# Kernel optimization log

Hardware: AMD Instinct MI355X
Metric: run time of the kernel (lower is better)

Reference implementation:

```python
import jax, jax.numpy as jnp
import numpy as np

C = 128        # in_channels
N = 80000      # nodes per type (user, item)
E = 1000000    # edges per relation
L = 400000     # link labels


def _evolve_gcn(x_src, edge_index, n_dst, p, W0, Wih, Whh, bih, bhh):
    """EvolveGCNH layer: TopK pooling -> 1-step GRU weight evolution -> GCN."""
    # TopK pooling: score = x @ p / ||p||, keep top C nodes, gate by tanh(score)
    score = x_src @ p / (jnp.linalg.norm(p) + 1e-16)          # [N_src]
    top_vals, top_idx = jax.lax.top_k(score, x_src.shape[1])   # k = C
    X_tilde = x_src[top_idx] * jnp.tanh(top_vals)[:, None]     # [C, C]
    # One GRU step: 'batch' dim = C rows of X_tilde, hidden = current weight W0
    gi = X_tilde @ Wih.T + bih                                 # [C, 3C]
    gh = W0 @ Whh.T + bhh                                      # [C, 3C]
    i_r, i_z, i_n = jnp.split(gi, 3, axis=1)
    h_r, h_z, h_n = jnp.split(gh, 3, axis=1)
    r = jax.nn.sigmoid(i_r + h_r)
    z = jax.nn.sigmoid(i_z + h_z)
    n = jnp.tanh(i_n + r * h_n)
    W = (1.0 - z) * n + z * W0                                 # evolved weight [C, C]
    # GCN propagation with symmetric degree norm, no self loops
    xw = x_src @ W                                             # [N_src, C]
    row, col = edge_index[0], edge_index[1]
    ones = jnp.ones(row.shape[0], dtype=xw.dtype)
    deg_src = jax.ops.segment_sum(ones, row, num_segments=x_src.shape[0])
    deg_dst = jax.ops.segment_sum(ones, col, num_segments=n_dst)
    inv_s = jnp.where(deg_src > 0, jax.lax.rsqrt(jnp.maximum(deg_src, 1.0)), 0.0)
    inv_d = jnp.where(deg_dst > 0, jax.lax.rsqrt(jnp.maximum(deg_dst, 1.0)), 0.0)
    norm = inv_s[row] * inv_d[col]                             # [E]
    return jax.ops.segment_sum(xw[row] * norm[:, None], col, num_segments=n_dst)


def setup_inputs() -> dict:
    key = jax.random.key(0)
    ks = jax.random.split(key, 20)
    f = lambda i, shape, s: jax.random.normal(ks[i], shape, dtype=jnp.float32) * s
    s_w = 1.0 / np.sqrt(C)
    return {
        "x_user": f(0, (N, C), 1.0),
        "x_item": f(1, (N, C), 1.0),
        "edge_ui": jax.random.randint(ks[2], (2, E), 0, N),
        "edge_iu": jax.random.randint(ks[3], (2, E), 0, N),
        "edge_label_index": jax.random.randint(ks[4], (2, L), 0, N),
        "p_ui": f(5, (C,), s_w),
        "W0_ui": f(6, (C, C), s_w),
        "Wih_ui": f(7, (3 * C, C), s_w),
        "Whh_ui": f(8, (3 * C, C), s_w),
        "bih_ui": f(9, (3 * C,), s_w),
        "bhh_ui": f(10, (3 * C,), s_w),
        "p_iu": f(11, (C,), s_w),
        "W0_iu": f(12, (C, C), s_w),
        "Wih_iu": f(13, (3 * C, C), s_w),
        "Whh_iu": f(14, (3 * C, C), s_w),
        "bih_iu": f(15, (3 * C,), s_w),
        "bhh_iu": f(16, (3 * C,), s_w),
        "W_post": f(17, (C, 2), s_w),
        "b_post": f(18, (2,), s_w),
    }


def reference(x_user, x_item, edge_ui, edge_iu, edge_label_index,
              p_ui, W0_ui, Wih_ui, Whh_ui, bih_ui, bhh_ui,
              p_iu, W0_iu, Wih_iu, Whh_iu, bih_iu, bhh_iu,
              W_post, b_post):
    # HeteroConv: one EvolveGCNH per relation, outputs grouped by dst node type
    h_item = jax.nn.relu(_evolve_gcn(x_user, edge_ui, x_item.shape[0],
                                     p_ui, W0_ui, Wih_ui, Whh_ui, bih_ui, bhh_ui))
    h_user = jax.nn.relu(_evolve_gcn(x_item, edge_iu, x_user.shape[0],
                                     p_iu, W0_iu, Wih_iu, Whh_iu, bih_iu, bhh_iu))
    # Link scorer: gather endpoints, hadamard, linear(C->2), sum over last dim
    h_src = h_user[edge_label_index[0]]                        # [L, C]
    h_dst = h_item[edge_label_index[1]]                        # [L, C]
    h = (h_src * h_dst) @ W_post + b_post                      # [L, 2]
    return jnp.sum(h, axis=-1)                                 # [L]
```

## Files before the change

kernel.cpp:

```cpp
#include <hip/hip_runtime.h>
#include <hip/hip_fp16.h>

constexpr int KC    = 128;
constexpr int NBLK  = 2048;
constexpr int CAPA  = 1024;
constexpr int CBITS = 10;
constexpr int CSZ   = 1 << CBITS;
constexpr int NBCM  = 192;

using half8   = __attribute__((ext_vector_type(8))) _Float16;
using float4v = __attribute__((ext_vector_type(4))) float;

__device__ __forceinline__ unsigned fkey(float s) {
  unsigned u = __float_as_uint(s);
  return (u & 0x80000000u) ? ~u : (u | 0x80000000u);
}

__global__ __launch_bounds__(256) void m1_cnt_scores(
    const int* __restrict__ eui, const int* __restrict__ eiu,
    unsigned* __restrict__ cnts, int* __restrict__ deg_src,
    const float* __restrict__ xu, const float* __restrict__ xi,
    const float* __restrict__ pu, const float* __restrict__ pi,
    float* __restrict__ scores, unsigned* __restrict__ hist,
    __half* __restrict__ x16,
    int E, int N, int NBC, int chunk) {
  __shared__ unsigned hD[4 * NBCM];
  int t = threadIdx.x;
  if (blockIdx.x < NBLK) {
    int blk = blockIdx.x, w = t >> 6;
    for (int b = t; b < 4 * NBCM; b += 256) hD[b] = 0;
    __syncthreads();
    int lo = blk * chunk, hi = min(2 * E, lo + chunk);
    for (int i = lo + t; i < hi; i += 256) {
      int rel = i >= E;
      const int* e = rel ? eiu : eui;
      int j = i - rel * E;
      atomicAdd(&hD[w * NBCM + ((rel * N + e[E + j]) >> CBITS)], 1u);
      atomicAdd(&deg_src[rel * N + e[j]], 1);
    }
    __syncthreads();
    for (int b = t; b < NBC; b += 256)
      cnts[(size_t)blk * NBC + b] =
          hD[b] + hD[NBCM + b] + hD[2 * NBCM + b] + hD[3 * NBCM + b];
  } else {
    int gw = (blockIdx.x - NBLK) * 8 + (t >> 5);
    if (gw >= 2 * N) return;
    int lane = t & 31;
    int rel = gw >= N;
    int r = gw - rel * N;
    const float* x = rel ? xi : xu;
    const float* p = rel ? pi : pu;
    float4 xv = ((const float4*)(x + (size_t)r * KC))[lane];
    float4 pv = ((const float4*)p)[lane];
    __half2 h0 = __floats2half2_rn(xv.x, xv.y);
    __half2 h1 = __floats2half2_rn(xv.z, xv.w);
    uint2 u; u.x = *(unsigned*)&h0; u.y = *(unsigned*)&h1;
    ((uint2*)(x16 + (size_t)gw * KC))[lane] = u;
    float s = xv.x * pv.x + xv.y * pv.y + xv.z * pv.z + xv.w * pv.w;
#pragma unroll
    for (int off = 16; off; off >>= 1) s += __shfl_down(s, off, 32);
    if (lane == 0) {
      scores[gw] = s;
      atomicAdd(&hist[rel * 65536 + (fkey(s) >> 16)], 1u);
    }
  }
}

__global__ __launch_bounds__(1024) void m2_thresh_scan1(
    const unsigned* __restrict__ cnts, unsigned* __restrict__ sc,
    unsigned* __restrict__ bsum, const unsigned* __restrict__ hist,
    unsigned* __restrict__ ctrl, int NTOT, int NBC) {
  __shared__ __align__(16) unsigned smem[1024 + 64 + 2];
  int t = threadIdx.x;
  if (blockIdx.x < 2) {
    const unsigned* h = hist + blockIdx.x * 65536;
    unsigned* c = ctrl + blockIdx.x * 8;
    unsigned* csum = smem;
    unsigned* bs = smem + 1024;
    unsigned s = 0;
    int hi = 65536 - 64 * t;
    for (int b = hi - 64; b < hi; ++b) s += h[b];
    csum[t] = s;
    __syncthreads();
    for (int off = 1; off < 1024; off <<= 1) {
      unsigned add = (t >= off) ? csum[t - off] : 0;
      __syncthreads();
      csum[t] += add;
      __syncthreads();
    }
    unsigned above = (t == 0) ? 0u : csum[t - 1];
    if (csum[t] >= 128u && above < 128u) { smem[1088] = (unsigned)t; smem[1089] = above; }
    __syncthreads();
    int chi = 65536 - 64 * (int)smem[1088];
    unsigned s_above = smem[1089];
    if (t < 64) bs[t] = h[chi - 1 - t];
    __syncthreads();
    if (t < 64) {
      unsigned v = bs[t], cum = v;
#pragma unroll
      for (int off = 1; off < 64; off <<= 1) {
        unsigned u = __shfl_up(cum, off, 64);
        if (t >= off) cum += u;
      }
      unsigned prev = cum - v;
      if (s_above + cum >= 128u && s_above + prev < 128u)
        c[0] = (unsigned)(chi - 1 - t);
    }
  } else {
    int vb = blockIdx.x - 2;
    unsigned* sh = smem;
    int li = vb * 1024 + t;
    unsigned v = 0;
    if (li < NTOT) {
      int b = li >> 11, blk = li & (NBLK - 1);
      v = cnts[(size_t)blk * NBC + b];
    }
    sh[t] = v; __syncthreads();
    for (int off = 1; off < 1024; off <<= 1) {
      unsigned add = (t >= off) ? sh[t - off] : 0;
      __syncthreads();
      sh[t] += add;
      __syncthreads();
    }
    if (li < NTOT) sc[li] = sh[t] - v;
    if (t == 1023) bsum[vb] = sh[1023];
  }
}

__global__ __launch_bounds__(512) void m3_scan2_compact(
    unsigned* __restrict__ bsum, int nb,
    const float* __restrict__ scores, unsigned* __restrict__ ctrl,
    int* __restrict__ cand_idx, float* __restrict__ cand_val, int N) {
  if (blockIdx.x == 0) {
    __shared__ unsigned sh[512];
    int t = threadIdx.x;
    unsigned v = (t < nb) ? bsum[t] : 0;
    sh[t] = v; __syncthreads();
    for (int off = 1; off < 512; off <<= 1) {
      unsigned add = (t >= off) ? sh[t - off] : 0;
      __syncthreads();
      sh[t] += add;
      __syncthreads();
    }
    if (t < nb) bsum[t] = sh[t] - v;
  } else {
    int i = (blockIdx.x - 1) * 512 + threadIdx.x;
    if (i >= 2 * N) return;
    int rel = i >= N;
    float s = scores[i];
    if ((fkey(s) >> 16) >= ctrl[rel * 8]) {
      unsigned pos = atomicAdd(&ctrl[rel * 8 + 1], 1u);
      if (pos < 2048u) {
        cand_idx[rel * 2048 + pos] = i - rel * N;
        cand_val[rel * 2048 + pos] = s;
      }
    }
  }
}

__global__ __launch_bounds__(256) void m4_topk_part(
    const int* __restrict__ eui, const int* __restrict__ eiu,
    const unsigned* __restrict__ cnts, const unsigned* __restrict__ sc,
    const unsigned* __restrict__ bsum,
    unsigned* __restrict__ recsD,
    const unsigned* __restrict__ ctrl,
    const int* __restrict__ cand_idx, const float* __restrict__ cand_val,
    const float* __restrict__ pu, const float* __restrict__ pi,
    int* __restrict__ top_idx, float* __restrict__ top_tanh,
    int E, int N, int NBC, int chunk) {
  __shared__ __align__(16) char smem[16896];
  int t = threadIdx.x;
  if (blockIdx.x < 2) {
    float* vals = (float*)smem;
    int*   idxs = (int*)(smem + 8192);
    float* red  = (float*)(smem + 16384);
    int rel = blockIdx.x;
    const float* p = rel ? pi : pu;
    int n = (int)ctrl[rel * 8 + 1]; if (n > 2048) n = 2048;
    for (int i = t; i < n; i += 256) {
      vals[i] = cand_val[rel * 2048 + i];
      idxs[i] = cand_idx[rel * 2048 + i];
    }
    if (t < 128) { float pv = p[t]; red[t] = pv * pv; }
    __syncthreads();
    for (int off = 64; off; off >>= 1) {
      if (t < off) red[t] += red[t + off];
      __syncthreads();
    }
    float pn = sqrtf(red[0]) + 1e-16f;
    for (int c = t; c < n; c += 256) {
      float v = vals[c]; int id = idxs[c];
      int rank = 0;
      for (int j = 0; j < n; ++j) {
        float vj = vals[j];
        rank += (vj > v) || (vj == v && idxs[j] < id);
      }
      if (rank < KC) {
        top_idx[rel * KC + rank] = id;
        top_tanh[rel * KC + rank] = tanhf(v / pn);
      }
    }
  } else {
    unsigned* scn    = (unsigned*)smem;
    unsigned* curD   = (unsigned*)(smem + 1024);
    unsigned* deltaD = (unsigned*)(smem + 2048);
    unsigned* stageD = (unsigned*)(smem + 3072);
    unsigned char* bktD = (unsigned char*)(smem + 7168);
    int blk = blockIdx.x - 2;
    unsigned v = (t < NBC) ? cnts[(size_t)blk * NBC + t] : 0;
    scn[t] = v; __syncthreads();
    for (int off = 1; off < 256; off <<= 1) {
      unsigned add = (t >= off) ? scn[t - off] : 0;
      __syncthreads();
      scn[t] += add;
      __syncthreads();
    }
    if (t < NBC) {
      unsigned exc = scn[t] - v;
      curD[t] = exc;
      int li = t * NBLK + blk;
      deltaD[t] = sc[li] + bsum[li >> 10] - exc;
    }
    __syncthreads();
    int lo = blk * chunk, hi = min(2 * E, lo + chunk);
    for (int i = lo + t; i < hi; i += 256) {
      int rel = i >= E;
      const int* e = rel ? eiu : eui;
      int j = i - rel * E;
      int src_g = rel * N + e[j];
      int dst_g = rel * N + e[E + j];
      int bD = dst_g >> CBITS;
      unsigned pD = atomicAdd(&curD[bD], 1u);
      stageD[pD] = (unsigned)src_g | ((unsigned)(dst_g & (CSZ - 1)) << 18);
      bktD[pD] = (unsigned char)bD;
    }
    __syncthreads();
    int cnt = hi - lo;
    for (int j = t; j < cnt; j += 256)
      recsD[deltaD[bktD[j]] + j] = stageD[j];
  }
}

__global__ __launch_bounds__(1024) void m5_refine_gru(
    const unsigned* __restrict__ sc, const unsigned* __restrict__ bsum,
    const unsigned* __restrict__ recsD,
    int* __restrict__ ssrc, int* __restrict__ deg_dst, int* __restrict__ endp,
    const float* __restrict__ xu, const float* __restrict__ xi,
    const int* __restrict__ top_idx, const float* __restrict__ top_tanh,
    const float* __restrict__ W0u, const float* __restrict__ W0i,
    const float* __restrict__ Wihu, const float* __restrict__ Wihi,
    const float* __restrict__ Whhu, const float* __restrict__ Whhi,
    const float* __restrict__ bihu, const float* __restrict__ bihi,
    const float* __restrict__ bhhu, const float* __restrict__ bhhi,
    __half* __restrict__ Wt,
    int E, int NBC, int N2) {
  __shared__ __align__(16) char smem[8256];
  int t = threadIdx.x;
  if ((int)blockIdx.x < NBC) {
    unsigned* hist = (unsigned*)smem;
    unsigned* cur  = (unsigned*)(smem + 4096);
    unsigned* t16  = (unsigned*)(smem + 8192);
    int c = blockIdx.x;
    int liLo = c * NBLK;
    int lo = (int)(sc[liLo] + bsum[liLo >> 10]);
    int hi;
    if (c + 1 < NBC) {
      int liHi = (c + 1) * NBLK;
      hi = (int)(sc[liHi] + bsum[liHi >> 10]);
    } else hi = 2 * E;
    hist[t] = 0;
    __syncthreads();
    for (int j = lo + t; j < hi; j += 1024)
      atomicAdd(&hist[recsD[j] >> 18], 1u);
    __syncthreads();
    unsigned v = hist[t];
    unsigned inc = v;
#pragma unroll
    for (int off = 1; off < 64; off <<= 1) {
      unsigned u = __shfl_up(inc, off, 64);
      if ((t & 63) >= off) inc += u;
    }
    int w = t >> 6;
    if ((t & 63) == 63) t16[w] = inc;
    __syncthreads();
    unsigned wbase = 0;
    for (int j = 0; j < 16; ++j) if (j < w) wbase += t16[j];
    unsigned exc = wbase + inc - v;
    cur[t] = exc;
    int node = c * CSZ + t;
    if (node < N2) {
      deg_dst[node] = (int)v;
      endp[node] = lo + (int)(exc + v);
    }
    __syncthreads();
    for (int j = lo + t; j < hi; j += 1024) {
      unsigned rec = recsD[j];
      unsigned pos = atomicAdd(&cur[rec >> 18], 1u);
      ssrc[lo + (int)pos] = (int)(rec & 0x3FFFFu);
    }
  } else {
    int gb = blockIdx.x - NBC;
    int rel = gb >> 7, c = gb & 127;
    const float* x   = rel ? xi   : xu;
    const float* W0  = rel ? W0i  : W0u;
    const float* Wih = rel ? Wihi : Wihu;
    const float* Whh = rel ? Whhi : Whhu;
    const float* bih = rel ? bihi : bihu;
    const float* bhh = rel ? bhhi : bhhu;
    float* xt = (float*)smem;
    float* w0 = (float*)(smem + 512);
    if (t < KC) {
      xt[t] = x[(size_t)top_idx[rel * KC + c] * KC + t] * top_tanh[rel * KC + c];
      w0[t] = W0[c * KC + t];
    }
    __syncthreads();
    if (t >= KC) return;
    int k = t;
    float gir = bih[k], giz = bih[KC + k], gin = bih[2 * KC + k];
    float ghr = bhh[k], ghz = bhh[KC + k], ghn = bhh[2 * KC + k];
    const float* wr = Wih + (size_t)k * KC;
    const float* wz = Wih + (size_t)(KC + k) * KC;
    const float* wn = Wih + (size_t)(2 * KC + k) * KC;
    const float* vr = Whh + (size_t)k * KC;
    const float* vz = Whh + (size_t)(KC + k) * KC;
    const float* vn = Whh + (size_t)(2 * KC + k) * KC;
    for (int j = 0; j < KC; ++j) {
      float xj = xt[j], hj = w0[j];
      gir += xj * wr[j]; giz += xj * wz[j]; gin += xj * wn[j];
      ghr += hj * vr[j]; ghz += hj * vz[j]; ghn += hj * vn[j];
    }
    float r = 1.f / (1.f + expf(-(gir + ghr)));
    float z = 1.f / (1.f + expf(-(giz + ghz)));
    float nn = tanhf(gin + r * ghn);
    float w = (1.f - z) * nn + z * w0[k];
    Wt[(size_t)rel * KC * KC + (size_t)k * KC + c] = __float2half_rn(w);
  }
}

__global__ __launch_bounds__(256) void k_gemm(const __half* __restrict__ x16,
                                              const __half* __restrict__ Wt,
                                              const int* __restrict__ deg_src,
                                              __half* __restrict__ xw, int N) {
  __shared__ __half Ws[KC * KC];
  __shared__ __half outs[64 * 136];
  int rel = (blockIdx.x * 64) >= N;
  int t = threadIdx.x;
  const uint4* wg = (const uint4*)(Wt + (size_t)rel * KC * KC);
#pragma unroll
  for (int i = 0; i < 8; ++i)
    ((uint4*)Ws)[t + 256 * i] = wg[t + 256 * i];
  __syncthreads();
  int wid = t >> 6, lane = t & 63;
  int l15 = lane & 15, quad = lane >> 4;
  int row0 = blockIdx.x * 64 + wid * 16;
  half8 a[4];
  const __half* xrow = x16 + (size_t)(row0 + l15) * KC + quad * 8;
#pragma unroll
  for (int ks = 0; ks < 4; ++ks) a[ks] = *(const half8*)(xrow + ks * 32);
  float4v acc[8];
#pragma unroll
  for (int nt = 0; nt < 8; ++nt) {
    acc[nt] = (float4v){0.f, 0.f, 0.f, 0.f};
#pragma unroll
    for (int ks = 0; ks < 4; ++ks) {
      half8 b = *(const half8*)&Ws[(nt * 16 + l15) * KC + ks * 32 + quad * 8];
      acc[nt] = __builtin_amdgcn_mfma_f32_16x16x32_f16(a[ks], b, acc[nt], 0, 0, 0);
    }
  }
  float scv[4];
#pragma unroll
  for (int r = 0; r < 4; ++r) {
    int dg = deg_src[row0 + quad * 4 + r];
    scv[r] = dg > 0 ? rsqrtf((float)dg) : 0.f;
  }
  __half* ob = outs + (size_t)wid * 16 * 136;
#pragma unroll
  for (int nt = 0; nt < 8; ++nt)
#pragma unroll
    for (int r = 0; r < 4; ++r)
      ob[(quad * 4 + r) * 136 + nt * 16 + l15] = __float2half_rn(acc[nt][r] * scv[r]);
  __syncthreads();
  size_t gbase = (size_t)blockIdx.x * 64 * KC;
#pragma unroll
  for (int i = 0; i < 4; ++i) {
    int idx = t + 256 * i;
    int rr = idx >> 4, cc = idx & 15;
    *(uint4*)(xw + gbase + (size_t)rr * KC + cc * 8) =
        *(const uint4*)(outs + (size_t)rr * 136 + cc * 8);
  }
}

__global__ void k_agg(const __half* __restrict__ xw, const int* __restrict__ ssrc,
                      const int* __restrict__ endp, const int* __restrict__ deg_dst,
                      __half* __restrict__ h, int n2) {
  int gw = (int)((blockIdx.x * blockDim.x + threadIdx.x) >> 6);
  if (gw >= n2) return;
  int lane = threadIdx.x & 63;
  int q = lane >> 4, l16 = lane & 15;
  int d = deg_dst[gw];
  int end = endp[gw], start = end - d;
  __half2 z = __floats2half2_rn(0.f, 0.f);
  __half2 a0[4], a1[4], a2[4], a3[4];
#pragma unroll
  for (int k = 0; k < 4; ++k) { a0[k] = z; a1[k] = z; a2[k] = z; a3[k] = z; }
  for (int i = start + q; i < end; i += 16) {
    int i1 = i + 4, i2 = i + 8, i3 = i + 12;
    bool b1 = i1 < end, b2 = i2 < end, b3 = i3 < end;
    int r0 = ssrc[i], r1, r2, r3;
    if (b1) r1 = ssrc[i1];
    if (b2) r2 = ssrc[i2];
    if (b3) r3 = ssrc[i3];
    uint4 u0 = ((const uint4*)(xw + (size_t)r0 * KC))[l16];
    uint4 u1, u2, u3;
    if (b1) u1 = ((const uint4*)(xw + (size_t)r1 * KC))[l16];
    if (b2) u2 = ((const uint4*)(xw + (size_t)r2 * KC))[l16];
    if (b3) u3 = ((const uint4*)(xw + (size_t)r3 * KC))[l16];
    {
      const __half2* p = (const __half2*)&u0;
#pragma unroll
      for (int k = 0; k < 4; ++k) a0[k] = __hadd2(a0[k], p[k]);
    }
    if (b1) {
      const __half2* p = (const __half2*)&u1;
#pragma unroll
      for (int k = 0; k < 4; ++k) a1[k] = __hadd2(a1[k], p[k]);
    }
    if (b2) {
      const __half2* p = (const __half2*)&u2;
#pragma unroll
      for (int k = 0; k < 4; ++k) a2[k] = __hadd2(a2[k], p[k]);
    }
    if (b3) {
      const __half2* p = (const __half2*)&u3;
#pragma unroll
      for (int k = 0; k < 4; ++k) a3[k] = __hadd2(a3[k], p[k]);
    }
  }
  float f[8];
#pragma unroll
  for (int k = 0; k < 4; ++k) {
    float2 x0 = __half22float2(a0[k]);
    float2 x1 = __half22float2(a1[k]);
    float2 x2 = __half22float2(a2[k]);
    float2 x3 = __half22float2(a3[k]);
    f[2 * k]     = (x0.x + x1.x) + (x2.x + x3.x);
    f[2 * k + 1] = (x0.y + x1.y) + (x2.y + x3.y);
  }
#pragma unroll
  for (int k = 0; k < 8; ++k) {
    f[k] += __shfl_xor(f[k], 16, 64);
    f[k] += __shfl_xor(f[k], 32, 64);
  }
  if (q == 0) {
    float invd = d > 0 ? rsqrtf((float)d) : 0.f;
    __half2 pk[4];
#pragma unroll
    for (int k = 0; k < 4; ++k)
      pk[k] = __floats2half2_rn(fmaxf(f[2 * k] * invd, 0.f),
                                fmaxf(f[2 * k + 1] * invd, 0.f));
    uint4 u;
    u.x = *(unsigned*)&pk[0]; u.y = *(unsigned*)&pk[1];
    u.z = *(unsigned*)&pk[2]; u.w = *(unsigned*)&pk[3];
    ((uint4*)(h + (size_t)gw * KC))[l16] = u;
  }
}

__global__ void k_links(const __half* __restrict__ h,
                        const int* __restrict__ srcs, const int* __restrict__ dsts,
                        const float* __restrict__ Wp, const float* __restrict__ bp,
                        float* __restrict__ out, int L, int N) {
  int tid = blockIdx.x * blockDim.x + threadIdx.x;
  int lane = threadIdx.x & 63;
  int q = lane >> 4, l16 = lane & 15;
  int gq = (tid >> 6) * 4 + q;
  int nq = (int)((gridDim.x * blockDim.x) >> 6) * 4;
  float w8[8];
#pragma unroll
  for (int k = 0; k < 4; ++k) {
    float4 w = ((const float4*)Wp)[l16 * 4 + k];
    w8[2 * k] = w.x + w.y; w8[2 * k + 1] = w.z + w.w;
  }
  float bs = bp[0] + bp[1];
  const __half* hu = h + (size_t)N * KC;
  for (int li = gq; li < L; li += nq) {
    int s = srcs[li], dd = dsts[li];
    uint4 ua = ((const uint4*)(hu + (size_t)s * KC))[l16];
    uint4 ub = ((const uint4*)(h + (size_t)dd * KC))[l16];
    const __half2* pa = (const __half2*)&ua;
    const __half2* pb = (const __half2*)&ub;
    float acc = 0.f;
#pragma unroll
    for (int k = 0; k < 4; ++k) {
      float2 fa = __half22float2(pa[k]);
      float2 fb = __half22float2(pb[k]);
      acc += fa.x * fb.x * w8[2 * k] + fa.y * fb.y * w8[2 * k + 1];
    }
#pragma unroll
    for (int off = 8; off; off >>= 1) acc += __shfl_xor(acc, off, 64);
    if (l16 == 0) out[li] = acc + bs;
  }
}

extern "C" void kernel_launch(void* const* d_in, const int* in_sizes, int n_in,
                              void* d_out, int out_size, void* d_ws, size_t ws_size,
                              hipStream_t stream) {
  const float* x_user = (const float*)d_in[0];
  const float* x_item = (const float*)d_in[1];
  const int*   edge_ui = (const int*)d_in[2];
  const int*   edge_iu = (const int*)d_in[3];
  const int*   elab    = (const int*)d_in[4];
  const float* p_ui   = (const float*)d_in[5];
  const float* W0_ui  = (const float*)d_in[6];
  const float* Wih_ui = (const float*)d_in[7];
  const float* Whh_ui = (const float*)d_in[8];
  const float* bih_ui = (const float*)d_in[9];
  const float* bhh_ui = (const float*)d_in[10];
  const float* p_iu   = (const float*)d_in[11];
  const float* W0_iu  = (const float*)d_in[12];
  const float* Wih_iu = (const float*)d_in[13];
  const float* Whh_iu = (const float*)d_in[14];
  const float* bih_iu = (const float*)d_in[15];
  const float* bhh_iu = (const float*)d_in[16];
  const float* W_post = (const float*)d_in[17];
  const float* b_post = (const float*)d_in[18];
  const int N = in_sizes[0] / KC;
  const int E = in_sizes[2] / 2;
  const int L = in_sizes[4] / 2;
  const int N2 = 2 * N;
  const int NBC = (N2 + CSZ - 1) >> CBITS;
  const int chunk = (2 * E + NBLK - 1) / NBLK;
  const int NTOT = NBC * NBLK;
  const int SCB = (NTOT + 1023) / 1024;

  char* wsp = (char*)d_ws;
  auto carve = [&](size_t bytes) -> void* {
    void* p = (void*)wsp;
    wsp += (bytes + 255) & ~(size_t)255;
    return p;
  };
  const size_t histB = 2 * 65536 * 4;
  const size_t zBytes = histB + 256 + (size_t)N2 * 4;
  char*     zbase    = (char*)carve(zBytes);
  unsigned* hist     = (unsigned*)zbase;
  unsigned* ctrl     = (unsigned*)(zbase + histB);
  int*      deg_src  = (int*)(zbase + histB + 256);
  __half*   x16      = (__half*)carve((size_t)N2 * KC * 2);
  __half*   xw       = (__half*)carve((size_t)N2 * KC * 2);
  __half*   h        = (__half*)carve((size_t)N2 * KC * 2);
  float*    scores   = (float*)carve((size_t)N2 * 4);
  int*      cand_idx = (int*)carve(2 * 2048 * 4);
  float*    cand_val = (float*)carve(2 * 2048 * 4);
  int*      top_idx  = (int*)carve(2 * KC * 4);
  float*    top_tanh = (float*)carve(2 * KC * 4);
  __half*   Wt16     = (__half*)carve(2 * KC * KC * 2);
  unsigned* cnts     = (unsigned*)carve((size_t)NTOT * 4);
  unsigned* sc       = (unsigned*)carve((size_t)NTOT * 4);
  unsigned* bsum     = (unsigned*)carve((size_t)SCB * 4);
  unsigned* recsD    = (unsigned*)carve((size_t)2 * E * 4);
  int*      ssrc     = (int*)carve((size_t)2 * E * 4);
  int*      deg_dst  = (int*)carve((size_t)N2 * 4);
  int*      endp     = (int*)carve((size_t)N2 * 4);

  hipMemsetAsync(zbase, 0, zBytes, stream);

  const int SBLK = (N2 + 7) / 8;
  m1_cnt_scores<<<NBLK + SBLK, 256, 0, stream>>>(edge_ui, edge_iu, cnts, deg_src,
                                                 x_user, x_item, p_ui, p_iu,
                                                 scores, hist, x16,
                                                 E, N, NBC, chunk);
  m2_thresh_scan1<<<2 + SCB, 1024, 0, stream>>>(cnts, sc, bsum, hist, ctrl,
                                                NTOT, NBC);
  m3_scan2_compact<<<1 + (N2 + 511) / 512, 512, 0, stream>>>(bsum, SCB, scores, ctrl,
                                                             cand_idx, cand_val, N);
  m4_topk_part<<<2 + NBLK, 256, 0, stream>>>(edge_ui, edge_iu, cnts, sc, bsum,
                                             recsD, ctrl, cand_idx, cand_val,
                                             p_ui, p_iu, top_idx, top_tanh,
                                             E, N, NBC, chunk);
  m5_refine_gru<<<NBC + 2 * KC, 1024, 0, stream>>>(sc, bsum, recsD, ssrc,
                                                   deg_dst, endp,
                                                   x_user, x_item, top_idx, top_tanh,
                                                   W0_ui, W0_iu, Wih_ui, Wih_iu,
                                                   Whh_ui, Whh_iu, bih_ui, bih_iu,
                                                   bhh_ui, bhh_iu, Wt16,
                                                   E, NBC, N2);
  k_gemm<<<N2 / 64, 256, 0, stream>>>(x16, Wt16, deg_src, xw, N);
  k_agg<<<(N2 + 3) / 4, 256, 0, stream>>>(xw, ssrc, endp, deg_dst, h, N2);
  k_links<<<2048, 256, 0, stream>>>(h, elab, elab + L, W_post, b_post,
                                    (float*)d_out, L, N);
}
```

Baseline: 458.4 us.

## Compute source degrees via bucketed partition instead of global atomics

Replaces the 2M global atomicAdds into deg_src with a second counting-sort partition keyed by source bucket. Block histograms are scanned alongside the destination ones, 16-bit local source ids are scattered into recsS, and per-bucket shared-memory histograms in m5 then write deg_src directly. This removes contended global atomics and the memset of deg_src. In exchange it adds an extra scan pass, an extra 4MB scatter write and readback, and more shared memory in m4.

Result: faster. 396.5 us (-13.5%).

```diff
diff --git a/kernel.cpp b/kernel.cpp
--- a/kernel.cpp
+++ b/kernel.cpp
@@ -18,17 +18,17 @@
 
 __global__ __launch_bounds__(256) void m1_cnt_scores(
     const int* __restrict__ eui, const int* __restrict__ eiu,
-    unsigned* __restrict__ cnts, int* __restrict__ deg_src,
+    unsigned* __restrict__ cnts,
     const float* __restrict__ xu, const float* __restrict__ xi,
     const float* __restrict__ pu, const float* __restrict__ pi,
     float* __restrict__ scores, unsigned* __restrict__ hist,
     __half* __restrict__ x16,
-    int E, int N, int NBC, int chunk) {
-  __shared__ unsigned hD[4 * NBCM];
+    int E, int N, int NBC, int chunk, int NTOT) {
+  __shared__ unsigned hD[4 * NBCM], hS[4 * NBCM];
   int t = threadIdx.x;
   if (blockIdx.x < NBLK) {
     int blk = blockIdx.x, w = t >> 6;
-    for (int b = t; b < 4 * NBCM; b += 256) hD[b] = 0;
+    for (int b = t; b < 4 * NBCM; b += 256) { hD[b] = 0; hS[b] = 0; }
     __syncthreads();
     int lo = blk * chunk, hi = min(2 * E, lo + chunk);
     for (int i = lo + t; i < hi; i += 256) {
@@ -36,12 +36,15 @@
       const int* e = rel ? eiu : eui;
       int j = i - rel * E;
       atomicAdd(&hD[w * NBCM + ((rel * N + e[E + j]) >> CBITS)], 1u);
-      atomicAdd(&deg_src[rel * N + e[j]], 1);
-    }
-    __syncthreads();
-    for (int b = t; b < NBC; b += 256)
+      atomicAdd(&hS[w * NBCM + ((rel * N + e[j]) >> CBITS)], 1u);
+    }
+    __syncthreads();
+    for (int b = t; b < NBC; b += 256) {
       cnts[(size_t)blk * NBC + b] =
           hD[b] + hD[NBCM + b] + hD[2 * NBCM + b] + hD[3 * NBCM + b];
+      cnts[(size_t)NTOT + (size_t)blk * NBC + b] =
+          hS[b] + hS[NBCM + b] + hS[2 * NBCM + b] + hS[3 * NBCM + b];
+    }
   } else {
     int gw = (blockIdx.x - NBLK) * 8 + (t >> 5);
     if (gw >= 2 * N) return;
@@ -69,7 +72,7 @@
 __global__ __launch_bounds__(1024) void m2_thresh_scan1(
     const unsigned* __restrict__ cnts, unsigned* __restrict__ sc,
     unsigned* __restrict__ bsum, const unsigned* __restrict__ hist,
-    unsigned* __restrict__ ctrl, int NTOT, int NBC) {
+    unsigned* __restrict__ ctrl, int NTOT, int NBC, int SCB) {
   __shared__ __align__(16) unsigned smem[1024 + 64 + 2];
   int t = threadIdx.x;
   if (blockIdx.x < 2) {
@@ -109,11 +112,12 @@
   } else {
     int vb = blockIdx.x - 2;
     unsigned* sh = smem;
-    int li = vb * 1024 + t;
+    int seg = vb / SCB, lb = vb % SCB;
+    int li = lb * 1024 + t;
     unsigned v = 0;
     if (li < NTOT) {
       int b = li >> 11, blk = li & (NBLK - 1);
-      v = cnts[(size_t)blk * NBC + b];
+      v = cnts[(size_t)seg * NTOT + (size_t)blk * NBC + b];
     }
     sh[t] = v; __syncthreads();
     for (int off = 1; off < 1024; off <<= 1) {
@@ -122,7 +126,7 @@
       sh[t] += add;
       __syncthreads();
     }
-    if (li < NTOT) sc[li] = sh[t] - v;
+    if (li < NTOT) sc[(size_t)seg * NTOT + li] = sh[t] - v;
     if (t == 1023) bsum[vb] = sh[1023];
   }
 }
@@ -131,10 +135,11 @@
     unsigned* __restrict__ bsum, int nb,
     const float* __restrict__ scores, unsigned* __restrict__ ctrl,
     int* __restrict__ cand_idx, float* __restrict__ cand_val, int N) {
-  if (blockIdx.x == 0) {
+  if (blockIdx.x < 2) {
     __shared__ unsigned sh[512];
+    unsigned* bs = bsum + blockIdx.x * nb;
     int t = threadIdx.x;
-    unsigned v = (t < nb) ? bsum[t] : 0;
+    unsigned v = (t < nb) ? bs[t] : 0;
     sh[t] = v; __syncthreads();
     for (int off = 1; off < 512; off <<= 1) {
       unsigned add = (t >= off) ? sh[t - off] : 0;
@@ -142,9 +147,9 @@
       sh[t] += add;
       __syncthreads();
     }
-    if (t < nb) bsum[t] = sh[t] - v;
+    if (t < nb) bs[t] = sh[t] - v;
   } else {
-    int i = (blockIdx.x - 1) * 512 + threadIdx.x;
+    int i = (blockIdx.x - 2) * 512 + threadIdx.x;
     if (i >= 2 * N) return;
     int rel = i >= N;
     float s = scores[i];
@@ -162,12 +167,12 @@
     const int* __restrict__ eui, const int* __restrict__ eiu,
     const unsigned* __restrict__ cnts, const unsigned* __restrict__ sc,
     const unsigned* __restrict__ bsum,
-    unsigned* __restrict__ recsD,
+    unsigned* __restrict__ recsD, unsigned short* __restrict__ recsS,
     const unsigned* __restrict__ ctrl,
     const int* __restrict__ cand_idx, const float* __restrict__ cand_val,
     const float* __restrict__ pu, const float* __restrict__ pi,
     int* __restrict__ top_idx, float* __restrict__ top_tanh,
-    int E, int N, int NBC, int chunk) {
+    int E, int N, int NBC, int chunk, int NTOT, int SCB) {
   __shared__ __align__(16) char smem[16896];
   int t = threadIdx.x;
   if (blockIdx.x < 2) {
@@ -203,12 +208,16 @@
   } else {
     unsigned* scn    = (unsigned*)smem;
     unsigned* curD   = (unsigned*)(smem + 1024);
-    unsigned* deltaD = (unsigned*)(smem + 2048);
-    unsigned* stageD = (unsigned*)(smem + 3072);
-    unsigned char* bktD = (unsigned char*)(smem + 7168);
+    unsigned* curS   = (unsigned*)(smem + 2048);
+    unsigned* deltaD = (unsigned*)(smem + 3072);
+    unsigned* deltaS = (unsigned*)(smem + 4096);
+    unsigned* stageD = (unsigned*)(smem + 5120);
+    unsigned short* stageS = (unsigned short*)(smem + 9216);
+    unsigned char* bktD = (unsigned char*)(smem + 11264);
+    unsigned char* bktS = (unsigned char*)(smem + 12288);
     int blk = blockIdx.x - 2;
-    unsigned v = (t < NBC) ? cnts[(size_t)blk * NBC + t] : 0;
-    scn[t] = v; __syncthreads();
+    unsigned vD = (t < NBC) ? cnts[(size_t)blk * NBC + t] : 0;
+    scn[t] = vD; __syncthreads();
     for (int off = 1; off < 256; off <<= 1) {
       unsigned add = (t >= off) ? scn[t - off] : 0;
       __syncthreads();
@@ -216,10 +225,25 @@
       __syncthreads();
     }
     if (t < NBC) {
-      unsigned exc = scn[t] - v;
+      unsigned exc = scn[t] - vD;
       curD[t] = exc;
       int li = t * NBLK + blk;
       deltaD[t] = sc[li] + bsum[li >> 10] - exc;
+    }
+    __syncthreads();
+    unsigned vS = (t < NBC) ? cnts[(size_t)NTOT + (size_t)blk * NBC + t] : 0;
+    scn[t] = vS; __syncthreads();
+    for (int off = 1; off < 256; off <<= 1) {
+      unsigned add = (t >= off) ? scn[t - off] : 0;
+      __syncthreads();
+      scn[t] += add;
+      __syncthreads();
+    }
+    if (t < NBC) {
+      unsigned exc = scn[t] - vS;
+      curS[t] = exc;
+      int li = t * NBLK + blk;
+      deltaS[t] = sc[NTOT + li] + bsum[SCB + (li >> 10)] - exc;
     }
     __syncthreads();
     int lo = blk * chunk, hi = min(2 * E, lo + chunk);
@@ -233,18 +257,25 @@
       unsigned pD = atomicAdd(&curD[bD], 1u);
       stageD[pD] = (unsigned)src_g | ((unsigned)(dst_g & (CSZ - 1)) << 18);
       bktD[pD] = (unsigned char)bD;
+      int bS = src_g >> CBITS;
+      unsigned pS = atomicAdd(&curS[bS], 1u);
+      stageS[pS] = (unsigned short)(src_g & (CSZ - 1));
+      bktS[pS] = (unsigned char)bS;
     }
     __syncthreads();
     int cnt = hi - lo;
-    for (int j = t; j < cnt; j += 256)
+    for (int j = t; j < cnt; j += 256) {
       recsD[deltaD[bktD[j]] + j] = stageD[j];
+      recsS[deltaS[bktS[j]] + j] = stageS[j];
+    }
   }
 }
 
 __global__ __launch_bounds__(1024) void m5_refine_gru(
     const unsigned* __restrict__ sc, const unsigned* __restrict__ bsum,
-    const unsigned* __restrict__ recsD,
+    const unsigned* __restrict__ recsD, const unsigned short* __restrict__ recsS,
     int* __restrict__ ssrc, int* __restrict__ deg_dst, int* __restrict__ endp,
+    int* __restrict__ deg_src,
     const float* __restrict__ xu, const float* __restrict__ xi,
     const int* __restrict__ top_idx, const float* __restrict__ top_tanh,
     const float* __restrict__ W0u, const float* __restrict__ W0i,
@@ -253,7 +284,7 @@
     const float* __restrict__ bihu, const float* __restrict__ bihi,
     const float* __restrict__ bhhu, const float* __restrict__ bhhi,
     __half* __restrict__ Wt,
-    int E, int NBC, int N2) {
+    int E, int NBC, int N2, int NTOT, int SCB) {
   __shared__ __align__(16) char smem[8256];
   int t = threadIdx.x;
   if ((int)blockIdx.x < NBC) {
@@ -298,8 +329,25 @@
       unsigned pos = atomicAdd(&cur[rec >> 18], 1u);
       ssrc[lo + (int)pos] = (int)(rec & 0x3FFFFu);
     }
+  } else if ((int)blockIdx.x < 2 * NBC) {
+    unsigned* hist = (unsigned*)smem;
+    int c = blockIdx.x - NBC;
+    int liLo = c * NBLK;
+    int lo = (int)(sc[NTOT + liLo] + bsum[SCB + (liLo >> 10)]);
+    int hi;
+    if (c + 1 < NBC) {
+      int liHi = (c + 1) * NBLK;
+      hi = (int)(sc[NTOT + liHi] + bsum[SCB + (liHi >> 10)]);
+    } else hi = 2 * E;
+    hist[t] = 0;
+    __syncthreads();
+    for (int j = lo + t; j < hi; j += 1024)
+      atomicAdd(&hist[(unsigned)recsS[j]], 1u);
+    __syncthreads();
+    int node = c * CSZ + t;
+    if (node < N2) deg_src[node] = (int)hist[t];
   } else {
-    int gb = blockIdx.x - NBC;
+    int gb = blockIdx.x - 2 * NBC;
     int rel = gb >> 7, c = gb & 127;
     const float* x   = rel ? xi   : xu;
     const float* W0  = rel ? W0i  : W0u;
@@ -539,11 +587,11 @@
     return p;
   };
   const size_t histB = 2 * 65536 * 4;
-  const size_t zBytes = histB + 256 + (size_t)N2 * 4;
+  const size_t zBytes = histB + 256;
   char*     zbase    = (char*)carve(zBytes);
   unsigned* hist     = (unsigned*)zbase;
   unsigned* ctrl     = (unsigned*)(zbase + histB);
-  int*      deg_src  = (int*)(zbase + histB + 256);
+  int*      deg_src  = (int*)carve((size_t)N2 * 4);
   __half*   x16      = (__half*)carve((size_t)N2 * KC * 2);
   __half*   xw       = (__half*)carve((size_t)N2 * KC * 2);
   __half*   h        = (__half*)carve((size_t)N2 * KC * 2);
@@ -553,10 +601,11 @@
   int*      top_idx  = (int*)carve(2 * KC * 4);
   float*    top_tanh = (float*)carve(2 * KC * 4);
   __half*   Wt16     = (__half*)carve(2 * KC * KC * 2);
-  unsigned* cnts     = (unsigned*)carve((size_t)NTOT * 4);
-  unsigned* sc       = (unsigned*)carve((size_t)NTOT * 4);
-  unsigned* bsum     = (unsigned*)carve((size_t)SCB * 4);
+  unsigned* cnts     = (unsigned*)carve((size_t)2 * NTOT * 4);
+  unsigned* sc       = (unsigned*)carve((size_t)2 * NTOT * 4);
+  unsigned* bsum     = (unsigned*)carve((size_t)2 * SCB * 4);
   unsigned* recsD    = (unsigned*)carve((size_t)2 * E * 4);
+  unsigned short* recsS = (unsigned short*)carve((size_t)2 * E * 2);
   int*      ssrc     = (int*)carve((size_t)2 * E * 4);
   int*      deg_dst  = (int*)carve((size_t)N2 * 4);
   int*      endp     = (int*)carve((size_t)N2 * 4);
@@ -564,25 +613,25 @@
   hipMemsetAsync(zbase, 0, zBytes, stream);
 
   const int SBLK = (N2 + 7) / 8;
-  m1_cnt_scores<<<NBLK + SBLK, 256, 0, stream>>>(edge_ui, edge_iu, cnts, deg_src,
+  m1_cnt_scores<<<NBLK + SBLK, 256, 0, stream>>>(edge_ui, edge_iu, cnts,
                                                  x_user, x_item, p_ui, p_iu,
                                                  scores, hist, x16,
-                                                 E, N, NBC, chunk);
-  m2_thresh_scan1<<<2 + SCB, 1024, 0, stream>>>(cnts, sc, bsum, hist, ctrl,
-                                                NTOT, NBC);
-  m3_scan2_compact<<<1 + (N2 + 511) / 512, 512, 0, stream>>>(bsum, SCB, scores, ctrl,
+                                                 E, N, NBC, chunk, NTOT);
+  m2_thresh_scan1<<<2 + 2 * SCB, 1024, 0, stream>>>(cnts, sc, bsum, hist, ctrl,
+                                                    NTOT, NBC, SCB);
+  m3_scan2_compact<<<2 + (N2 + 511) / 512, 512, 0, stream>>>(bsum, SCB, scores, ctrl,
                                                              cand_idx, cand_val, N);
   m4_topk_part<<<2 + NBLK, 256, 0, stream>>>(edge_ui, edge_iu, cnts, sc, bsum,
-                                             recsD, ctrl, cand_idx, cand_val,
+                                             recsD, recsS, ctrl, cand_idx, cand_val,
                                              p_ui, p_iu, top_idx, top_tanh,
-                                             E, N, NBC, chunk);
-  m5_refine_gru<<<NBC + 2 * KC, 1024, 0, stream>>>(sc, bsum, recsD, ssrc,
-                                                   deg_dst, endp,
-                                                   x_user, x_item, top_idx, top_tanh,
-                                                   W0_ui, W0_iu, Wih_ui, Wih_iu,
-                                                   Whh_ui, Whh_iu, bih_ui, bih_iu,
-                                                   bhh_ui, bhh_iu, Wt16,
-                                                   E, NBC, N2);
+                                             E, N, NBC, chunk, NTOT, SCB);
+  m5_refine_gru<<<2 * NBC + 2 * KC, 1024, 0, stream>>>(sc, bsum, recsD, recsS, ssrc,
+                                                       deg_dst, endp, deg_src,
+                                                       x_user, x_item, top_idx, top_tanh,
+                                                       W0_ui, W0_iu, Wih_ui, Wih_iu,
+                                                       Whh_ui, Whh_iu, bih_ui, bih_iu,
+                                                       bhh_ui, bhh_iu, Wt16,
+                                                       E, NBC, N2, NTOT, SCB);
   k_gemm<<<N2 / 64, 256, 0, stream>>>(x16, Wt16, deg_src, xw, N);
   k_agg<<<(N2 + 3) / 4, 256, 0, stream>>>(xw, ssrc, endp, deg_dst, h, N2);
   k_links<<<2048, 256, 0, stream>>>(h, elab, elab + L, W_post, b_post,
```
